# Kernel tuning notes

Measured on AMD Instinct MI355X. Metric: run time of the kernel, lower is better.

The kernel has to match this reference:

```python
import jax, jax.numpy as jnp
import numpy as np

H = 32
DECAY = 0.9


def setup_inputs() -> dict:
    key = jax.random.key(0)
    ks = jax.random.split(key, 6)
    B, T, D = 8, 4096, 1024
    x = jax.random.normal(ks[0], (B, T, D), dtype=jnp.float32)
    s = 1.0 / np.sqrt(D)
    Wv = jax.random.normal(ks[1], (D, D), dtype=jnp.float32) * s
    bv = jax.random.normal(ks[2], (D,), dtype=jnp.float32) * s
    Wo = jax.random.normal(ks[3], (D, D), dtype=jnp.float32) * s
    bo = jax.random.normal(ks[4], (D,), dtype=jnp.float32) * s
    w = jnp.asarray(DECAY ** np.arange(H), dtype=jnp.float32)
    decay_w = w / jnp.sum(w)
    return {"x": x, "Wv": Wv, "bv": bv, "Wo": Wo, "bo": bo, "decay_w": decay_w}


def reference(x, Wv, bv, Wo, bo, decay_w):
    # x: [B, T, D]. Original pads H zeros at front and unfolds windows of size H
    # with stride 1, producing T+1 windows: window t covers x[t-H .. t-1].
    # value_proj is linear and applied to every window copy, so it commutes with
    # the fixed-weight sum: attended = (sum_i w_i * x_window_i) @ Wv^T + bv*sum(w).
    B, T, D = x.shape
    Hlen = decay_w.shape[0]
    x_pad = jnp.pad(x, ((0, 0), (Hlen, 0), (0, 0)))  # [B, T+H, D]
    # Depthwise 1D conv over time with the (shared) decay kernel.
    kernel = jnp.broadcast_to(decay_w[:, None, None], (Hlen, 1, D))  # [W, I=1, O=D]
    s = jax.lax.conv_general_dilated(
        x_pad, kernel, window_strides=(1,), padding="VALID",
        dimension_numbers=("NWC", "WIO", "NWC"), feature_group_count=D,
    )  # [B, T+1, D]
    attended = s @ Wv.T + bv * jnp.sum(decay_w)
    return attended @ Wo.T + bo  # [B, T+1, D]
```

## Files before the change

### kernel.cpp

```cpp
#include <hip/hip_runtime.h>
#include <stdint.h>

#define D_DIM 1024
#define T_DIM 4096
#define B_DIM 8
#define M_REAL (B_DIM * (T_DIM + 1))
#define M_MAIN 32768
#define NWG 512

typedef short short8 __attribute__((ext_vector_type(8)));
typedef float floatx4 __attribute__((ext_vector_type(4)));

typedef const __attribute__((address_space(1))) void* gptr_t;
typedef __attribute__((address_space(3))) void* lptr_t;

__device__ __forceinline__ ushort f2bf(float f) {
  union { float f; uint32_t u; } v; v.f = f;
  uint32_t r = v.u + 0x7FFF + ((v.u >> 16) & 1);
  return (ushort)(r >> 16);
}
__device__ __forceinline__ float bf2f(ushort b) {
  union { uint32_t u; float f; } v; v.u = ((uint32_t)b) << 16; return v.f;
}

#define BARRIER()  asm volatile("s_barrier" ::: "memory")
#define WAIT_VM2() asm volatile("s_waitcnt vmcnt(2)" ::: "memory")
#define WAIT_VM0() asm volatile("s_waitcnt vmcnt(0)" ::: "memory")
#define WAIT_LGKM0() do { asm volatile("s_waitcnt lgkmcnt(0)" ::: "memory"); \
                          __builtin_amdgcn_sched_barrier(0); } while (0)
#define SP1() __builtin_amdgcn_s_setprio(1)
#define SP0() __builtin_amdgcn_s_setprio(0)

__global__ __launch_bounds__(1024) void gemm_w16_kernel(
    const ushort* __restrict__ A, const ushort* __restrict__ Bm,
    float* __restrict__ C, const float* __restrict__ bias)
{
  __shared__ char smem[65536];
  const int tid  = threadIdx.x;
  const int wave = tid >> 6;
  const int lane = tid & 63;
  const int wm = wave >> 2, wn = wave & 3;
  const int l15 = lane & 15, lhi = lane >> 4;

  const int bid = blockIdx.x;
  const int wg  = (bid & 7) * 64 + (bid >> 3);
  const int n0 = (wg & 3) * 256;
  const int m0 = (wg >> 2) * 256;

  const int srow = tid >> 2;
  const int ksw  = ((tid & 3) ^ ((tid >> 3) & 3)) * 8;
  const ushort* Aq = A  + (size_t)(m0 + srow) * D_DIM + ksw;
  const ushort* Bq = Bm + (size_t)(n0 + srow) * D_DIM + ksw;

  const int xorc = (lhi ^ ((l15 >> 1) & 3)) * 16;
  const int aoff = (wm * 64 + l15) * 64 + xorc;
  const int boff = (wn * 64 + l15) * 64 + xorc;

  short8 a[4], b[4];
  floatx4 acc[4][4] = {};

#define STAGE_W(PA, PB, S) do { \
  __builtin_amdgcn_global_load_lds((gptr_t)(PA), \
      (lptr_t)(smem + (S) * 16384 + wave * 1024), 16, 0, 0); \
  __builtin_amdgcn_global_load_lds((gptr_t)(PB), \
      (lptr_t)(smem + 32768 + (S) * 16384 + wave * 1024), 16, 0, 0); \
} while (0)

#define LDAB_W(S) do { \
  _Pragma("unroll") \
  for (int m = 0; m < 4; ++m) \
    a[m] = *(const short8*)(smem + (S) * 16384 + aoff + m * 1024); \
  _Pragma("unroll") \
  for (int n = 0; n < 4; ++n) \
    b[n] = *(const short8*)(smem + 32768 + (S) * 16384 + boff + n * 1024); \
} while (0)

#define MFMA_W() do { \
  _Pragma("unroll") \
  for (int m = 0; m < 4; ++m) \
    _Pragma("unroll") \
    for (int n = 0; n < 4; ++n) \
      acc[m][n] = __builtin_amdgcn_mfma_f32_16x16x32_bf16( \
          a[m], b[n], acc[m][n], 0, 0, 0); \
} while (0)

#define ITER_W(S0, STG, VMW) do { \
  if (STG) { STAGE_W(ApS, BpS, (S0) ^ 1); ApS += 32; BpS += 32; } \
  VMW; \
  BARRIER(); \
  LDAB_W(S0); \
  WAIT_LGKM0(); \
  SP1(); MFMA_W(); SP0(); \
  BARRIER(); \
} while (0)

  STAGE_W(Aq, Bq, 0);
  const ushort* ApS = Aq + 32;
  const ushort* BpS = Bq + 32;

#pragma unroll 1
  for (int it = 0; it < 15; ++it) {
    ITER_W(0, 1, WAIT_VM2());
    ITER_W(1, 1, WAIT_VM2());
  }
  ITER_W(0, 1, WAIT_VM2());
  ITER_W(1, 0, WAIT_VM0());

#pragma unroll
  for (int m = 0; m < 4; ++m)
#pragma unroll
    for (int n = 0; n < 4; ++n) {
      const int gn = n0 + wn * 64 + n * 16 + l15;
      const float bia = bias[gn];
#pragma unroll
      for (int j = 0; j < 4; ++j) {
        const int gm = m0 + wm * 64 + m * 16 + lhi * 4 + j;
        C[(size_t)gm * D_DIM + gn] = acc[m][n][j] + bia;
      }
    }
#undef STAGE_W
#undef LDAB_W
#undef MFMA_W
#undef ITER_W
}

__global__ __launch_bounds__(256) void tail_gemv_kernel(
    const ushort* __restrict__ S, const ushort* __restrict__ Wf,
    const float* __restrict__ cvec, float* __restrict__ out)
{
  const int wavei = threadIdx.x >> 6, lane = threadIdx.x & 63;
  const int c = blockIdx.x * 4 + wavei;
  float acc[8] = {};
  for (int i = 0; i < 16; ++i) {
    const int k = i * 64 + lane;
    const float wv = bf2f(Wf[(size_t)c * D_DIM + k]);
#pragma unroll
    for (int r = 0; r < 8; ++r)
      acc[r] += wv * bf2f(S[(size_t)(M_MAIN + r) * D_DIM + k]);
  }
#pragma unroll
  for (int r = 0; r < 8; ++r) {
#pragma unroll
    for (int off = 32; off; off >>= 1) acc[r] += __shfl_xor(acc[r], off, 64);
  }
  if (lane == 0) {
    const float bia = cvec[c];
#pragma unroll
    for (int r = 0; r < 8; ++r)
      out[(size_t)(M_MAIN + r) * D_DIM + c] = acc[r] + bia;
  }
}

__global__ __launch_bounds__(256) void gemm_bt_kernel(
    const ushort* __restrict__ A, const ushort* __restrict__ Bm,
    ushort* __restrict__ Cb, int K, int N)
{
  __shared__ ushort As[128][64];
  __shared__ ushort Bs[128][64];
  const int tid  = threadIdx.x;
  const int wave = tid >> 6;
  const int lane = tid & 63;
  const int wm = wave >> 1, wn = wave & 1;
  const int n0 = blockIdx.x * 128, m0 = blockIdx.y * 128;
  const int l15 = lane & 15, lhi = lane >> 4;

  floatx4 acc[4][4] = {};

  const int srow = tid >> 3;
  const int sk8  = (tid & 7) * 8;
  const ushort* Ab = A  + (size_t)(m0 + srow) * K + sk8;
  const ushort* Bb = Bm + (size_t)(n0 + srow) * K + sk8;

  for (int k0 = 0; k0 < K; k0 += 64) {
#pragma unroll
    for (int q = 0; q < 4; ++q)
      __builtin_amdgcn_global_load_lds((gptr_t)(Ab + k0 + (size_t)q * 32 * K),
          (lptr_t)((char*)&As[0][0] + (q * 256 + wave * 64) * 16), 16, 0, 0);
#pragma unroll
    for (int q = 0; q < 4; ++q)
      __builtin_amdgcn_global_load_lds((gptr_t)(Bb + k0 + (size_t)q * 32 * K),
          (lptr_t)((char*)&Bs[0][0] + (q * 256 + wave * 64) * 16), 16, 0, 0);
    __syncthreads();

#pragma unroll
    for (int kk = 0; kk < 2; ++kk) {
      short8 af[4], bfrg[4];
#pragma unroll
      for (int i = 0; i < 4; ++i) {
        af[i]   = *(const short8*)(&As[wm * 64 + i * 16 + l15][kk * 32 + lhi * 8]);
        bfrg[i] = *(const short8*)(&Bs[wn * 64 + i * 16 + l15][kk * 32 + lhi * 8]);
      }
#pragma unroll
      for (int mi = 0; mi < 4; ++mi)
#pragma unroll
        for (int ni = 0; ni < 4; ++ni)
          acc[mi][ni] = __builtin_amdgcn_mfma_f32_16x16x32_bf16(
              af[mi], bfrg[ni], acc[mi][ni], 0, 0, 0);
    }
    __syncthreads();
  }

#pragma unroll
  for (int mi = 0; mi < 4; ++mi)
#pragma unroll
    for (int ni = 0; ni < 4; ++ni) {
      const int gn = n0 + wn * 64 + ni * 16 + l15;
#pragma unroll
      for (int j = 0; j < 4; ++j) {
        const int gm = m0 + wm * 64 + mi * 16 + lhi * 4 + j;
        Cb[(size_t)gm * N + gn] = f2bf(acc[mi][ni][j]);
      }
    }
}

#define CTCH 128
__global__ __launch_bounds__(256) void conv_kernel(
    const float* __restrict__ x, const float* __restrict__ dw,
    ushort* __restrict__ S)
{
  const int b   = blockIdx.y;
  const int col = blockIdx.z * 256 + threadIdx.x;
  const int t0  = blockIdx.x * CTCH;

  float w[32];
#pragma unroll
  for (int i = 0; i < 32; ++i) w[i] = dw[i];
  const float rinv = w[0] / w[1];
  const float w31  = w[31];
  const float c0   = -w[0] * rinv;

  const float* xb = x + (size_t)b * T_DIM * D_DIM + col;
  ushort*      Sb = S + (size_t)b * (T_DIM + 1) * D_DIM + col;

  float prev[32], cur[32];
  float s;
  if (blockIdx.x == 0) {
#pragma unroll
    for (int i = 0; i < 32; ++i) prev[i] = 0.f;
    s = 0.f;
    Sb[0] = f2bf(0.f);
  } else {
#pragma unroll
    for (int i = 0; i < 32; ++i) prev[i] = xb[(size_t)(t0 - 32 + i) * D_DIM];
    s = 0.f;
#pragma unroll
    for (int i = 0; i < 32; ++i) s = __builtin_fmaf(w[i], prev[i], s);
  }

#pragma unroll 1
  for (int g = 0; g < 4; g += 2) {
#pragma unroll
    for (int i = 0; i < 32; ++i) cur[i] = xb[(size_t)(t0 + g * 32 + i) * D_DIM];
#pragma unroll
    for (int j = 0; j < 32; ++j) {
      s = __builtin_fmaf(s, rinv, __builtin_fmaf(prev[j], c0, w31 * cur[j]));
      Sb[(size_t)(t0 + g * 32 + 1 + j) * D_DIM] = f2bf(s);
    }
    s = 0.f;
#pragma unroll
    for (int i = 0; i < 32; ++i) s = __builtin_fmaf(w[i], cur[i], s);
#pragma unroll
    for (int i = 0; i < 32; ++i) prev[i] = xb[(size_t)(t0 + (g + 1) * 32 + i) * D_DIM];
#pragma unroll
    for (int j = 0; j < 32; ++j) {
      s = __builtin_fmaf(s, rinv, __builtin_fmaf(cur[j], c0, w31 * prev[j]));
      Sb[(size_t)(t0 + (g + 1) * 32 + 1 + j) * D_DIM] = f2bf(s);
    }
    s = 0.f;
#pragma unroll
    for (int i = 0; i < 32; ++i) s = __builtin_fmaf(w[i], prev[i], s);
  }
}

__global__ void convert_wo_kernel(const float* __restrict__ Wo, ushort* __restrict__ WoB) {
  const int i = blockIdx.x * 256 + threadIdx.x;
  const float4 v = ((const float4*)Wo)[i];
  ushort4 o = make_ushort4(f2bf(v.x), f2bf(v.y), f2bf(v.z), f2bf(v.w));
  *(ushort4*)(WoB + (size_t)i * 4) = o;
}

__global__ void transpose_wv_kernel(const float* __restrict__ Wv, ushort* __restrict__ WvT) {
  __shared__ float tile[32][33];
  const int tx = threadIdx.x;
  const int ty = threadIdx.y;
  const int c0 = blockIdx.x * 32;
  const int r0 = blockIdx.y * 32;
#pragma unroll
  for (int j = 0; j < 4; ++j)
    tile[ty + j * 8][tx] = Wv[(size_t)(r0 + ty + j * 8) * D_DIM + c0 + tx];
  __syncthreads();
#pragma unroll
  for (int j = 0; j < 4; ++j)
    WvT[(size_t)(c0 + ty + j * 8) * D_DIM + r0 + tx] = f2bf(tile[tx][ty + j * 8]);
}

__global__ void bias_kernel(const float* __restrict__ Wo, const float* __restrict__ bv,
                            const float* __restrict__ bo, const float* __restrict__ dw,
                            float* __restrict__ cvec) {
  const int j    = blockIdx.x * 4 + (threadIdx.x >> 6);
  const int lane = threadIdx.x & 63;
  float sumw = 0.f;
#pragma unroll
  for (int i = 0; i < 32; ++i) sumw += dw[i];
  float s = 0.f;
  for (int k = lane; k < D_DIM; k += 64) s += Wo[(size_t)j * D_DIM + k] * bv[k];
#pragma unroll
  for (int off = 32; off; off >>= 1) s += __shfl_xor(s, off, 64);
  if (lane == 0) cvec[j] = sumw * s + bo[j];
}

extern "C" void kernel_launch(void* const* d_in, const int* in_sizes, int n_in,
                              void* d_out, int out_size, void* d_ws, size_t ws_size,
                              hipStream_t stream) {
  const float* x  = (const float*)d_in[0];
  const float* Wv = (const float*)d_in[1];
  const float* bv = (const float*)d_in[2];
  const float* Wo = (const float*)d_in[3];
  const float* bo = (const float*)d_in[4];
  const float* dw = (const float*)d_in[5];
  float* out = (float*)d_out;

  char* ws = (char*)d_ws;
  ushort* S      = (ushort*)ws;
  ushort* WoB    = (ushort*)(ws + (size_t)M_REAL * D_DIM * 2);
  ushort* WvT    = WoB + (size_t)D_DIM * D_DIM;
  ushort* Wfused = WvT + (size_t)D_DIM * D_DIM;
  float*  cvec   = (float*)(Wfused + (size_t)D_DIM * D_DIM);

  convert_wo_kernel<<<dim3(D_DIM * D_DIM / 1024), dim3(256), 0, stream>>>(Wo, WoB);
  transpose_wv_kernel<<<dim3(32, 32), dim3(32, 8), 0, stream>>>(Wv, WvT);
  bias_kernel<<<dim3(256), dim3(256), 0, stream>>>(Wo, bv, bo, dw, cvec);

  gemm_bt_kernel<<<dim3(8, 8), dim3(256), 0, stream>>>(
      WoB, WvT, Wfused, D_DIM, D_DIM);

  conv_kernel<<<dim3(T_DIM / CTCH, B_DIM, 4), dim3(256), 0, stream>>>(x, dw, S);

  gemm_w16_kernel<<<dim3(NWG), dim3(1024), 0, stream>>>(S, Wfused, out, cvec);
  tail_gemv_kernel<<<dim3(256), dim3(256), 0, stream>>>(S, Wfused, cvec, out);
}
```

Before: 165.5 us.

## Load B operand directly from global into registers, bypassing LDS

The GEMM kernel now keeps only the A tile in LDS via global_load_lds, while each wave loads its B fragments straight from global memory into double-buffered registers with inline asm dwordx4 loads. LDS use is halved and the per-iteration LDS reads for B are gone, which cuts LDS bandwidth and lowers the footprint that limits occupancy. In exchange, B is fetched redundantly by each wave row (4 waves share the same B columns), the loads are less coalesced (16-byte chunks over many rows), and register pressure goes up. The vmcnt wait depth is raised to account for the extra in-flight loads. Correctness depends on the asm loads being properly ordered by those vmcnt waits.

```diff
diff --git a/kernel.cpp b/kernel.cpp
--- a/kernel.cpp
+++ b/kernel.cpp
@@ -24,18 +24,20 @@
 }
 
 #define BARRIER()  asm volatile("s_barrier" ::: "memory")
-#define WAIT_VM2() asm volatile("s_waitcnt vmcnt(2)" ::: "memory")
+#define WAIT_VM5() asm volatile("s_waitcnt vmcnt(5)" ::: "memory")
 #define WAIT_VM0() asm volatile("s_waitcnt vmcnt(0)" ::: "memory")
 #define WAIT_LGKM0() do { asm volatile("s_waitcnt lgkmcnt(0)" ::: "memory"); \
                           __builtin_amdgcn_sched_barrier(0); } while (0)
 #define SP1() __builtin_amdgcn_s_setprio(1)
 #define SP0() __builtin_amdgcn_s_setprio(0)
+#define GLOAD16(DST, P) \
+  asm volatile("global_load_dwordx4 %0, %1, off" : "=v"(DST) : "v"(P) : "memory")
 
 __global__ __launch_bounds__(1024) void gemm_w16_kernel(
     const ushort* __restrict__ A, const ushort* __restrict__ Bm,
     float* __restrict__ C, const float* __restrict__ bias)
 {
-  __shared__ char smem[65536];
+  __shared__ char smem[32768];
   const int tid  = threadIdx.x;
   const int wave = tid >> 6;
   const int lane = tid & 63;
@@ -49,62 +51,64 @@
 
   const int srow = tid >> 2;
   const int ksw  = ((tid & 3) ^ ((tid >> 3) & 3)) * 8;
-  const ushort* Aq = A  + (size_t)(m0 + srow) * D_DIM + ksw;
-  const ushort* Bq = Bm + (size_t)(n0 + srow) * D_DIM + ksw;
+  const ushort* ApS = A + (size_t)(m0 + srow) * D_DIM + ksw;
 
   const int xorc = (lhi ^ ((l15 >> 1) & 3)) * 16;
   const int aoff = (wm * 64 + l15) * 64 + xorc;
-  const int boff = (wn * 64 + l15) * 64 + xorc;
-
-  short8 a[4], b[4];
+
+  const ushort* Bg = Bm + (size_t)(n0 + wn * 64 + l15) * D_DIM + lhi * 8;
+
+  short8 a[4];
+  short8 bA[4], bB[4];
   floatx4 acc[4][4] = {};
 
-#define STAGE_W(PA, PB, S) do { \
+#define STAGE_A(PA, S) \
   __builtin_amdgcn_global_load_lds((gptr_t)(PA), \
-      (lptr_t)(smem + (S) * 16384 + wave * 1024), 16, 0, 0); \
-  __builtin_amdgcn_global_load_lds((gptr_t)(PB), \
-      (lptr_t)(smem + 32768 + (S) * 16384 + wave * 1024), 16, 0, 0); \
+      (lptr_t)(smem + (S) * 16384 + wave * 1024), 16, 0, 0)
+
+#define BLOAD(SET, U) do { \
+  GLOAD16(SET[0], (Bg + (U) * 32)); \
+  GLOAD16(SET[1], (Bg + 16384 + (U) * 32)); \
+  GLOAD16(SET[2], (Bg + 32768 + (U) * 32)); \
+  GLOAD16(SET[3], (Bg + 49152 + (U) * 32)); \
 } while (0)
 
-#define LDAB_W(S) do { \
+#define LDA_W(S) do { \
   _Pragma("unroll") \
   for (int m = 0; m < 4; ++m) \
     a[m] = *(const short8*)(smem + (S) * 16384 + aoff + m * 1024); \
-  _Pragma("unroll") \
-  for (int n = 0; n < 4; ++n) \
-    b[n] = *(const short8*)(smem + 32768 + (S) * 16384 + boff + n * 1024); \
 } while (0)
 
-#define MFMA_W() do { \
+#define MFMA_W(BSET) do { \
   _Pragma("unroll") \
   for (int m = 0; m < 4; ++m) \
     _Pragma("unroll") \
     for (int n = 0; n < 4; ++n) \
       acc[m][n] = __builtin_amdgcn_mfma_f32_16x16x32_bf16( \
-          a[m], b[n], acc[m][n], 0, 0, 0); \
+          a[m], BSET[n], acc[m][n], 0, 0, 0); \
 } while (0)
 
-#define ITER_W(S0, STG, VMW) do { \
-  if (STG) { STAGE_W(ApS, BpS, (S0) ^ 1); ApS += 32; BpS += 32; } \
+#define ITER_W(S0, BCUR, BNXT, U1, STG, VMW) do { \
+  if (STG) { STAGE_A(ApS + (U1) * 32, (S0) ^ 1); BLOAD(BNXT, U1); } \
   VMW; \
   BARRIER(); \
-  LDAB_W(S0); \
+  LDA_W(S0); \
   WAIT_LGKM0(); \
-  SP1(); MFMA_W(); SP0(); \
+  SP1(); MFMA_W(BCUR); SP0(); \
   BARRIER(); \
 } while (0)
 
-  STAGE_W(Aq, Bq, 0);
-  const ushort* ApS = Aq + 32;
-  const ushort* BpS = Bq + 32;
+  STAGE_A(ApS, 0);
+  BLOAD(bA, 0);
 
 #pragma unroll 1
   for (int it = 0; it < 15; ++it) {
-    ITER_W(0, 1, WAIT_VM2());
-    ITER_W(1, 1, WAIT_VM2());
-  }
-  ITER_W(0, 1, WAIT_VM2());
-  ITER_W(1, 0, WAIT_VM0());
+    const int u = 2 * it;
+    ITER_W(0, bA, bB, u + 1, 1, WAIT_VM5());
+    ITER_W(1, bB, bA, u + 2, 1, WAIT_VM5());
+  }
+  ITER_W(0, bA, bB, 31, 1, WAIT_VM5());
+  ITER_W(1, bB, bA, 0, 0, WAIT_VM0());
 
 #pragma unroll
   for (int m = 0; m < 4; ++m)
@@ -118,8 +122,9 @@
         C[(size_t)gm * D_DIM + gn] = acc[m][n][j] + bia;
       }
     }
-#undef STAGE_W
-#undef LDAB_W
+#undef STAGE_A
+#undef BLOAD
+#undef LDA_W
 #undef MFMA_W
 #undef ITER_W
 }
```

Result: slower. 267.0 us (+61.3%).
